# Optimization experiments

Hardware: AMD Instinct MI355X
Metric: run time of the kernel (lower is better)

Reference implementation:

```python
import jax, jax.numpy as jnp
import numpy as np

B, S, D, H = 2, 2048, 512, 8
DK = D // H  # 64


def setup_inputs() -> dict:
    key = jax.random.key(0)
    ks = jax.random.split(key, 16)
    def t(k):
        return jax.random.normal(k, (B, S, D), dtype=jnp.float32)
    inp = {
        'query_real': t(ks[0]), 'key_real': t(ks[1]), 'value_real': t(ks[2]),
        'query_phase': t(ks[3]), 'key_phase': t(ks[4]), 'value_phase': t(ks[5]),
        'mask': jax.random.randint(ks[6], (B, 1, S), 0, 2, dtype=jnp.int32),
    }
    # Four distinct linear layers (clones deepcopies); real and phase paths share them.
    for i, nm in enumerate(['q', 'k', 'v', 'o']):
        inp['W' + nm] = jax.random.normal(ks[7 + 2 * i], (D, D), dtype=jnp.float32) * 0.02
        inp['b' + nm] = jax.random.normal(ks[8 + 2 * i], (D,), dtype=jnp.float32) * 0.02
    return inp


def _lin(x, W, b):
    # nn.Linear: x @ W.T + b
    return jnp.einsum('bsd,ed->bse', x, W) + b


def _heads(x):
    # [B,S,D] -> [B,H,S,DK]
    return jnp.swapaxes(x.reshape(B, S, H, DK), 1, 2)


def reference(query_real, key_real, value_real, query_phase, key_phase, value_phase,
              mask, Wq, bq, Wk, bk, Wv, bv, Wo, bo):
    qr = _heads(_lin(query_real, Wq, bq)); qp = _heads(_lin(query_phase, Wq, bq))
    kr = _heads(_lin(key_real, Wk, bk));   kp = _heads(_lin(key_phase, Wk, bk))
    vr = _heads(_lin(value_real, Wv, bv)); vp = _heads(_lin(value_phase, Wv, bv))

    # complex QK^T: 4 matmuls -> real/imag parts, magnitude score
    sr = jnp.einsum('bhqd,bhkd->bhqk', qr, kr) - jnp.einsum('bhqd,bhkd->bhqk', qp, kp)
    sp = jnp.einsum('bhqd,bhkd->bhqk', qr, kp) + jnp.einsum('bhqd,bhkd->bhqk', qp, kr)
    scores = jnp.sqrt(sr * sr + sp * sp) / jnp.sqrt(jnp.float32(DK))
    # mask [B,1,S] -> unsqueeze head dim -> [B,1,1,S]
    scores = jnp.where(mask[:, None] == 0, jnp.float32(-1e9), scores)
    p = jax.nn.softmax(scores, axis=-1)

    xr = jnp.einsum('bhqk,bhkd->bhqd', p, vr)
    xp = jnp.einsum('bhqk,bhkd->bhqd', p, vp)
    xr = jnp.swapaxes(xr, 1, 2).reshape(B, S, D)
    xp = jnp.swapaxes(xp, 1, 2).reshape(B, S, D)
    return _lin(xr, Wo, bo), _lin(xp, Wo, bo)
```

## Files before the change

### kernel.cpp

```cpp
#include <hip/hip_runtime.h>

typedef __bf16 bf16;
typedef __bf16 bf16x8 __attribute__((ext_vector_type(8)));
typedef float  f32x4  __attribute__((ext_vector_type(4)));

static constexpr int CB = 2;
static constexpr int CS = 2048;
static constexpr int CD = 512;
static constexpr int CH = 8;
static constexpr int CDK = 64;
static constexpr int NROWS = CB * CH * CS;
static constexpr size_t NT = (size_t)CB * CS * CD;
static constexpr size_t WN = (size_t)CD * CD;

__device__ __forceinline__ f32x4 mfma16(bf16x8 a, bf16x8 b, f32x4 c) {
    return __builtin_amdgcn_mfma_f32_16x16x32_bf16(a, b, c, 0, 0, 0);
}

__device__ __forceinline__ bf16x8 cvt8(const float* __restrict__ p) {
    float4 x0 = *reinterpret_cast<const float4*>(p);
    float4 x1 = *reinterpret_cast<const float4*>(p + 4);
    bf16x8 r;
    r[0] = (bf16)x0.x; r[1] = (bf16)x0.y; r[2] = (bf16)x0.z; r[3] = (bf16)x0.w;
    r[4] = (bf16)x1.x; r[5] = (bf16)x1.y; r[6] = (bf16)x1.z; r[7] = (bf16)x1.w;
    return r;
}

__device__ __forceinline__ void gload16(const void* g, void* l) {
    __builtin_amdgcn_global_load_lds(
        (const __attribute__((address_space(1))) void*)g,
        (__attribute__((address_space(3))) void*)l, 16, 0, 0);
}

struct CvtP {
    const float* src[10];
    bf16* dst[10];
    int n8[10];
};
__global__ __launch_bounds__(256) void cvt_kernel(CvtP C) {
    const int t = blockIdx.y;
    const int i = blockIdx.x * 256 + threadIdx.x;
    if (i < C.n8[t])
        *reinterpret_cast<bf16x8*>(C.dst[t] + (size_t)i * 8) =
            cvt8(C.src[t] + (size_t)i * 8);
}

struct PB {
    const bf16* A[6];
    const bf16* W[6];
    const float* bias[6];
    bf16* dst[6];
    int mode[6];
};
__global__ __launch_bounds__(256) void projb_kernel(PB P) {
    __shared__ uint4 tile[2][2][512];

    const int z = blockIdx.z;
    const bf16* __restrict__ A = P.A[z];
    const bf16* __restrict__ W = P.W[z];
    const float* __restrict__ bias = P.bias[z];
    bf16* __restrict__ dst = P.dst[z];
    const int mode = P.mode[z];

    const int m0 = blockIdx.x * 64, n0 = blockIdx.y * 64;
    const int tid = threadIdx.x;
    const int lane = tid & 63, w = tid >> 6;
    const int wm = w >> 1, wn = w & 1;
    const int l16 = lane & 15, lhi = lane >> 4;

    const int tensor = w >> 1, half = w & 1;
    const int rlo = lane >> 3, slotL = lane & 7;
    const bf16* gbase = tensor ? W : A;
    const int t0 = tensor ? n0 : m0;
    const char* gp = (const char*)gbase
                   + (size_t)(t0 + half*32 + rlo) * (CD * 2)
                   + (size_t)((slotL ^ rlo) * 16);

    auto stage = [&](int buf, int kk) {
        const char* p = gp + (size_t)kk * 128;
        uint4* ld = &tile[buf][tensor][half * 256];
        #pragma unroll
        for (int i = 0; i < 4; ++i)
            gload16(p + (size_t)i * 8 * (CD * 2), ld + i * 64);
    };

    f32x4 acc[2][2] = {};

    stage(0, 0);
    asm volatile("s_waitcnt vmcnt(0)" ::: "memory");
    __syncthreads();

    for (int kk = 0; kk < 8; ++kk) {
        if (kk + 1 < 8) stage((kk + 1) & 1, kk + 1);

        const uint4* aT = &tile[kk & 1][0][0];
        const uint4* bT = &tile[kk & 1][1][0];
        #pragma unroll
        for (int ks = 0; ks < 2; ++ks) {
            const int c = ks*4 + lhi;
            const int ra0 = wm*32 + l16, ra1 = ra0 + 16;
            const int rb0 = wn*32 + l16, rb1 = rb0 + 16;
            bf16x8 af0 = __builtin_bit_cast(bf16x8, aT[ra0*8 + (c ^ (ra0 & 7))]);
            bf16x8 af1 = __builtin_bit_cast(bf16x8, aT[ra1*8 + (c ^ (ra1 & 7))]);
            bf16x8 bg0 = __builtin_bit_cast(bf16x8, bT[rb0*8 + (c ^ (rb0 & 7))]);
            bf16x8 bg1 = __builtin_bit_cast(bf16x8, bT[rb1*8 + (c ^ (rb1 & 7))]);
            acc[0][0] = mfma16(af0, bg0, acc[0][0]);
            acc[0][1] = mfma16(af0, bg1, acc[0][1]);
            acc[1][0] = mfma16(af1, bg0, acc[1][0]);
            acc[1][1] = mfma16(af1, bg1, acc[1][1]);
        }
        if (kk + 1 < 8) __syncthreads();
    }

    #pragma unroll
    for (int ms = 0; ms < 2; ++ms)
    #pragma unroll
    for (int ns = 0; ns < 2; ++ns) {
        const int col = n0 + wn*32 + ns*16 + l16;
        const float bv = bias[col];
        const int hh = col >> 6, dk = col & 63;
        #pragma unroll
        for (int i = 0; i < 4; ++i) {
            const int m = m0 + wm*32 + ms*16 + lhi*4 + i;
            const float v = acc[ms][ns][i] + bv;
            const int b = m >> 11, s = m & 2047;
            if (mode == 0)
                dst[(((size_t)(b*CH + hh)) * CS + s) * CDK + dk] = (bf16)v;
            else
                dst[(((size_t)(b*CH + hh)) * CDK + dk) * CS + s] = (bf16)v;
        }
    }
}

__global__ __launch_bounds__(256) void oprojb_kernel(
    const bf16* __restrict__ Xr, const bf16* __restrict__ Xp,
    const bf16* __restrict__ Wo, const float* __restrict__ bo,
    float* __restrict__ out)
{
    __shared__ uint4 tile[2][2][512];

    const bf16* __restrict__ A = blockIdx.z ? Xp : Xr;
    float* __restrict__ dst = out + (size_t)blockIdx.z * NT;

    const int m0 = blockIdx.x * 64, n0 = blockIdx.y * 64;
    const int tid = threadIdx.x;
    const int lane = tid & 63, w = tid >> 6;
    const int wm = w >> 1, wn = w & 1;
    const int l16 = lane & 15, lhi = lane >> 4;

    const int tensor = w >> 1, half = w & 1;
    const int rlo = lane >> 3, slotL = lane & 7;
    const bf16* gbase = tensor ? Wo : A;
    const int t0 = tensor ? n0 : m0;
    const char* gp = (const char*)gbase
                   + (size_t)(t0 + half*32 + rlo) * (CD * 2)
                   + (size_t)((slotL ^ rlo) * 16);

    auto stage = [&](int buf, int kk) {
        const char* p = gp + (size_t)kk * 128;
        uint4* ld = &tile[buf][tensor][half * 256];
        #pragma unroll
        for (int i = 0; i < 4; ++i)
            gload16(p + (size_t)i * 8 * (CD * 2), ld + i * 64);
    };

    f32x4 acc[2][2] = {};

    stage(0, 0);
    asm volatile("s_waitcnt vmcnt(0)" ::: "memory");
    __syncthreads();

    for (int kk = 0; kk < 8; ++kk) {
        if (kk + 1 < 8) stage((kk + 1) & 1, kk + 1);

        const uint4* aT = &tile[kk & 1][0][0];
        const uint4* bT = &tile[kk & 1][1][0];
        #pragma unroll
        for (int ks = 0; ks < 2; ++ks) {
            const int c = ks*4 + lhi;
            const int ra0 = wm*32 + l16, ra1 = ra0 + 16;
            const int rb0 = wn*32 + l16, rb1 = rb0 + 16;
            bf16x8 af0 = __builtin_bit_cast(bf16x8, aT[ra0*8 + (c ^ (ra0 & 7))]);
            bf16x8 af1 = __builtin_bit_cast(bf16x8, aT[ra1*8 + (c ^ (ra1 & 7))]);
            bf16x8 bg0 = __builtin_bit_cast(bf16x8, bT[rb0*8 + (c ^ (rb0 & 7))]);
            bf16x8 bg1 = __builtin_bit_cast(bf16x8, bT[rb1*8 + (c ^ (rb1 & 7))]);
            acc[0][0] = mfma16(af0, bg0, acc[0][0]);
            acc[0][1] = mfma16(af0, bg1, acc[0][1]);
            acc[1][0] = mfma16(af1, bg0, acc[1][0]);
            acc[1][1] = mfma16(af1, bg1, acc[1][1]);
        }
        if (kk + 1 < 8) __syncthreads();
    }

    #pragma unroll
    for (int ms = 0; ms < 2; ++ms)
    #pragma unroll
    for (int ns = 0; ns < 2; ++ns) {
        const int col = n0 + wn*32 + ns*16 + l16;
        const float bv = bo[col];
        #pragma unroll
        for (int i = 0; i < 4; ++i) {
            const int m = m0 + wm*32 + ms*16 + lhi*4 + i;
            dst[(size_t)m * 512 + col] = acc[ms][ns][i] + bv;
        }
    }
}

__global__ __launch_bounds__(256) void attn_kernel(
    const bf16* __restrict__ Qr, const bf16* __restrict__ Qp,
    const bf16* __restrict__ Kr, const bf16* __restrict__ Kp,
    const bf16* __restrict__ Vtr, const bf16* __restrict__ Vtp,
    const int* __restrict__ mask, int lognsp,
    float* __restrict__ POR, float* __restrict__ POP, float* __restrict__ PLs)
{
    __shared__ uint4 stg[2][4][512];
    __shared__ bf16 pL[4][32][64];

    const int F = blockIdx.x;
    const int qt = (F >> 3) & 15;
    const int g  = (F & 7) | ((F >> 7) << 3);
    const int bh = g >> lognsp, z = g & ((1 << lognsp) - 1);
    const int Lkv = CS >> lognsp, kvbase = z * Lkv;
    const int nt = Lkv >> 6;
    const int b = bh >> 3;
    const size_t base = (size_t)bh * CS * CDK;

    const int tid = threadIdx.x, lane = tid & 63, w = tid >> 6;
    const int l16 = lane & 15, lhi = lane >> 4;
    const int q0 = qt * 128 + w * 32;

    const int srowL = lane >> 3, slotL = lane & 7;
    const int chunkL = slotL ^ srowL;
    const char* gsrc;
    size_t laneoff, iStride, tStride;
    if (w == 0)      gsrc = (const char*)Kr;
    else if (w == 1) gsrc = (const char*)Kp;
    else if (w == 2) gsrc = (const char*)Vtr;
    else             gsrc = (const char*)Vtp;
    if (w < 2) {
        laneoff = base*2 + (size_t)(kvbase + srowL) * 128 + chunkL*16;
        iStride = 1024;  tStride = 8192;
    } else {
        laneoff = base*2 + (size_t)srowL * (CS*2) + (size_t)kvbase*2 + chunkL*16;
        iStride = 8 * CS * 2;  tStride = 128;
    }
    const char* gp = gsrc + laneoff;

    auto stage = [&](int bi, int t) {
        const char* p = gp + (size_t)t * tStride;
        uint4* ldst = &stg[bi][w][0];
        #pragma unroll
        for (int i = 0; i < 8; ++i)
            gload16(p + i*iStride, ldst + i*64);
    };

    stage(0, 0);

    bf16x8 qrf[2][2], qpf[2][2], qnf[2][2];
    #pragma unroll
    for (int ms = 0; ms < 2; ++ms)
        #pragma unroll
        for (int ks = 0; ks < 2; ++ks) {
            const size_t qoff = base + (size_t)(q0 + ms*16 + l16) * CDK + ks*32 + lhi*8;
            qrf[ms][ks] = *reinterpret_cast<const bf16x8*>(&Qr[qoff]);
            qpf[ms][ks] = *reinterpret_cast<const bf16x8*>(&Qp[qoff]);
            uint4 t = __builtin_bit_cast(uint4, qpf[ms][ks]);
            t.x ^= 0x80008000u; t.y ^= 0x80008000u; t.z ^= 0x80008000u; t.w ^= 0x80008000u;
            qnf[ms][ks] = __builtin_bit_cast(bf16x8, t);
        }

    unsigned long long keep4[2] = {0ull, 0ull};
    for (int t = 0; t < nt; ++t) {
        const unsigned long long m64 =
            __ballot(mask[b*CS + kvbase + t*64 + lane] != 0);
        const unsigned long long bits = m64 >> l16;
        const unsigned long long nib =
            (bits & 1ull) | ((bits >> 15) & 2ull) | ((bits >> 30) & 4ull) | ((bits >> 45) & 8ull);
        keep4[t >> 4] |= nib << ((t & 15) * 4);
    }

    f32x4 oR[2][4] = {}, oP[2][4] = {};
    float lpart[2][4] = {};

    auto fswz = [](int r) { return (r & 7) ^ (((r >> 3) & 1) << 1); };

    asm volatile("s_waitcnt vmcnt(0)" ::: "memory");
    __syncthreads();

    for (int t = 0; t < nt; ++t) {
        if (t + 1 < nt) stage((t + 1) & 1, t + 1);

        const int bi = t & 1;
        const unsigned int k4 = (unsigned int)(keep4[t >> 4] >> ((t & 15) * 4)) & 0xFu;
        const uint4* kTr = &stg[bi][0][0];
        const uint4* kTp = &stg[bi][1][0];
        const uint4* vTr = &stg[bi][2][0];
        const uint4* vTp = &stg[bi][3][0];

        float sc[2][4][4];
        #pragma unroll
        for (int kb = 0; kb < 4; ++kb) {
            const int krow = kb*16 + l16;
            bf16x8 kr8[2], kp8[2];
            #pragma unroll
            for (int ks = 0; ks < 2; ++ks) {
                const int ci = krow*8 + ((ks*4 + lhi) ^ (krow & 7));
                kr8[ks] = __builtin_bit_cast(bf16x8, kTr[ci]);
                kp8[ks] = __builtin_bit_cast(bf16x8, kTp[ci]);
            }
            const unsigned int keep = (k4 >> kb) & 1u;
            #pragma unroll
            for (int ms = 0; ms < 2; ++ms) {
                f32x4 aR = {}, aP = {};
                __builtin_amdgcn_s_setprio(1);
                #pragma unroll
                for (int ks = 0; ks < 2; ++ks) {
                    aR = mfma16(qrf[ms][ks], kr8[ks], aR);
                    aR = mfma16(qnf[ms][ks], kp8[ks], aR);
                    aP = mfma16(qrf[ms][ks], kp8[ks], aP);
                    aP = mfma16(qpf[ms][ks], kr8[ks], aP);
                }
                __builtin_amdgcn_s_setprio(0);
                #pragma unroll
                for (int i = 0; i < 4; ++i) {
                    const float sr = aR[i], sp = aP[i];
                    const float mag = __builtin_amdgcn_sqrtf(fmaf(sr, sr, sp*sp));
                    float p = __builtin_amdgcn_exp2f(fmaf(mag, 0.18033688f, -5.77078016f));
                    p = keep ? p : 0.0f;
                    sc[ms][kb][i] = p;
                    lpart[ms][i] += p;
                }
            }
        }

        bf16* pB = &pL[w][0][0];
        #pragma unroll
        for (int ms = 0; ms < 2; ++ms)
            #pragma unroll
            for (int i = 0; i < 4; ++i) {
                const int row = ms*16 + lhi*4 + i;
                const int sw = fswz(row) << 3;
                #pragma unroll
                for (int kb = 0; kb < 4; ++kb)
                    pB[row*64 + ((kb*16 + l16) ^ sw)] = (bf16)sc[ms][kb][i];
            }
        asm volatile("s_waitcnt lgkmcnt(0)" ::: "memory");
        __builtin_amdgcn_sched_barrier(0);

        const uint4* pW = reinterpret_cast<const uint4*>(&pL[w][0][0]);
        #pragma unroll
        for (int ks = 0; ks < 2; ++ks) {
            bf16x8 pf[2];
            #pragma unroll
            for (int ms = 0; ms < 2; ++ms) {
                const int prow = ms*16 + l16;
                pf[ms] = __builtin_bit_cast(bf16x8, pW[prow*8 + ((ks*4 + lhi) ^ fswz(prow))]);
            }
            __builtin_amdgcn_s_setprio(1);
            #pragma unroll
            for (int d = 0; d < 4; ++d) {
                const int vrow = d*16 + l16;
                const int ci = vrow*8 + ((ks*4 + lhi) ^ (vrow & 7));
                const bf16x8 v8r = __builtin_bit_cast(bf16x8, vTr[ci]);
                const bf16x8 v8p = __builtin_bit_cast(bf16x8, vTp[ci]);
                #pragma unroll
                for (int ms = 0; ms < 2; ++ms) {
                    oR[ms][d] = mfma16(pf[ms], v8r, oR[ms][d]);
                    oP[ms][d] = mfma16(pf[ms], v8p, oP[ms][d]);
                }
            }
            __builtin_amdgcn_s_setprio(0);
        }

        if (t + 1 < nt) __syncthreads();
    }

    #pragma unroll
    for (int ms = 0; ms < 2; ++ms)
        #pragma unroll
        for (int i = 0; i < 4; ++i) {
            float v = lpart[ms][i];
            v += __shfl_xor(v, 1); v += __shfl_xor(v, 2);
            v += __shfl_xor(v, 4); v += __shfl_xor(v, 8);
            lpart[ms][i] = v;
        }
    const int r0 = bh * CS + q0;
    if (l16 == 0) {
        #pragma unroll
        for (int ms = 0; ms < 2; ++ms)
            #pragma unroll
            for (int i = 0; i < 4; ++i)
                PLs[(size_t)z * NROWS + r0 + ms*16 + lhi*4 + i] = lpart[ms][i];
    }
    const size_t zo = (size_t)z * NROWS * 64;
    #pragma unroll
    for (int ms = 0; ms < 2; ++ms)
        #pragma unroll
        for (int d = 0; d < 4; ++d) {
            const int col = d*16 + l16;
            #pragma unroll
            for (int i = 0; i < 4; ++i) {
                const size_t off = zo + (size_t)(r0 + ms*16 + lhi*4 + i) * 64 + col;
                POR[off] = oR[ms][d][i];
                POP[off] = oP[ms][d][i];
            }
        }
}

__global__ __launch_bounds__(256) void merge_kernel(
    const float* __restrict__ POR, const float* __restrict__ POP,
    const float* __restrict__ PLs, int nsp,
    bf16* __restrict__ Xr, bf16* __restrict__ Xp)
{
    const int idx = blockIdx.x * 256 + threadIdx.x;
    const int r = idx >> 4, c0 = (idx & 15) * 4;
    float l = 0.f;
    f32x4 orv = {}, opv = {};
    for (int zz = 0; zz < nsp; ++zz) {
        l += PLs[(size_t)zz * NROWS + r];
        const size_t o = (size_t)zz * NROWS * 64 + (size_t)r * 64 + c0;
        orv += *reinterpret_cast<const f32x4*>(&POR[o]);
        opv += *reinterpret_cast<const f32x4*>(&POP[o]);
    }
    const float inv = 1.f / l;
    const int bh = r >> 11, q = r & 2047;
    const int b = bh >> 3, h = bh & 7;
    const size_t off = ((size_t)(b*CS + q)) * CD + h*CDK + c0;
    bf16 vr[4], vp[4];
    #pragma unroll
    for (int j = 0; j < 4; ++j) { vr[j] = (bf16)(orv[j]*inv); vp[j] = (bf16)(opv[j]*inv); }
    *reinterpret_cast<uint2*>(&Xr[off]) = *reinterpret_cast<const uint2*>(vr);
    *reinterpret_cast<uint2*>(&Xp[off]) = *reinterpret_cast<const uint2*>(vp);
}

extern "C" void kernel_launch(void* const* d_in, const int* in_sizes, int n_in,
                              void* d_out, int out_size, void* d_ws, size_t ws_size,
                              hipStream_t stream) {
    const float* q_r = (const float*)d_in[0];
    const float* k_r = (const float*)d_in[1];
    const float* v_r = (const float*)d_in[2];
    const float* q_p = (const float*)d_in[3];
    const float* k_p = (const float*)d_in[4];
    const float* v_p = (const float*)d_in[5];
    const int*  mask = (const int*)d_in[6];
    const float* Wq = (const float*)d_in[7];  const float* bq = (const float*)d_in[8];
    const float* Wk = (const float*)d_in[9];  const float* bk = (const float*)d_in[10];
    const float* Wv = (const float*)d_in[11]; const float* bv = (const float*)d_in[12];
    const float* Wo = (const float*)d_in[13]; const float* bo = (const float*)d_in[14];
    float* out = (float*)d_out;

    bf16* ws = (bf16*)d_ws;
    bf16* Abf = ws;
    bf16* Wbf = ws + 6 * NT;
    bf16* Qr  = Wbf + 4 * WN;
    bf16 *Qp = Qr + NT, *Kr = Qp + NT, *Kp = Kr + NT;
    bf16 *Vtr = Kp + NT, *Vtp = Vtr + NT;
    bf16 *Xr = Vtp + NT, *Xp = Xr + NT;
    float* POR = (float*)(Xp + NT);

    const size_t fixedB = (14 * NT + 4 * WN) * sizeof(bf16);
    const size_t per_split = (size_t)NROWS * 64 * 4 * 2 + (size_t)NROWS * 4;
    int nsp, lognsp;
    if (ws_size >= fixedB + 2 * per_split) { nsp = 2; lognsp = 1; }
    else                                   { nsp = 1; lognsp = 0; }
    float* POP = POR + (size_t)nsp * NROWS * 64;
    float* PLs = POP + (size_t)nsp * NROWS * 64;

    dim3 blk(256);

    CvtP C;
    C.src[0]=q_r; C.src[1]=q_p; C.src[2]=k_r; C.src[3]=k_p; C.src[4]=v_r; C.src[5]=v_p;
    C.src[6]=Wq;  C.src[7]=Wk;  C.src[8]=Wv;  C.src[9]=Wo;
    for (int i = 0; i < 6; ++i) { C.dst[i] = Abf + (size_t)i * NT; C.n8[i] = (int)(NT / 8); }
    for (int i = 0; i < 4; ++i) { C.dst[6+i] = Wbf + (size_t)i * WN; C.n8[6+i] = (int)(WN / 8); }
    cvt_kernel<<<dim3((unsigned)(NT / 8 / 256), 10), blk, 0, stream>>>(C);

    PB P;
    for (int i = 0; i < 6; ++i) P.A[i] = Abf + (size_t)i * NT;
    P.W[0]=Wbf;      P.W[1]=Wbf;      P.W[2]=Wbf+WN;   P.W[3]=Wbf+WN;
    P.W[4]=Wbf+2*WN; P.W[5]=Wbf+2*WN;
    P.bias[0]=bq; P.bias[1]=bq; P.bias[2]=bk; P.bias[3]=bk; P.bias[4]=bv; P.bias[5]=bv;
    P.dst[0]=Qr; P.dst[1]=Qp; P.dst[2]=Kr; P.dst[3]=Kp; P.dst[4]=Vtr; P.dst[5]=Vtp;
    P.mode[0]=0; P.mode[1]=0; P.mode[2]=0; P.mode[3]=0; P.mode[4]=1; P.mode[5]=1;
    projb_kernel<<<dim3(64, 8, 6), blk, 0, stream>>>(P);

    attn_kernel<<<dim3(256 * nsp), blk, 0, stream>>>(Qr, Qp, Kr, Kp, Vtr, Vtp,
                                                     mask, lognsp, POR, POP, PLs);

    merge_kernel<<<dim3(NROWS * 16 / 256), blk, 0, stream>>>(POR, POP, PLs, nsp, Xr, Xp);

    oprojb_kernel<<<dim3(64, 8, 2), blk, 0, stream>>>(Xr, Xp, Wbf + 3 * WN, bo, out);
}
```

Before: 128.1 us.

## Compute transposed scores to keep P in registers, drop LDS round-trip

Swaps the MFMA operand order so the score tile comes out transposed, with keys along the accumulator rows. The probabilities can then be packed to bf16 and rearranged with permlane swaps straight into the B-operand layout for the PV MFMA, which removes the per-wave LDS staging buffer, its writes and reads, and the lgkmcnt wait. The mask bits are repacked per lane, and the output is now written as vectorized f32x4 stores. In exchange it relies on gfx950-specific permlane swap instructions and inline asm, and K fragments are reloaded from LDS for each ms instead of being reused.

Result: no change. 128.6 us (+0.4%).

```diff
diff --git a/kernel.cpp b/kernel.cpp
--- a/kernel.cpp
+++ b/kernel.cpp
@@ -214,7 +214,6 @@
     float* __restrict__ POR, float* __restrict__ POP, float* __restrict__ PLs)
 {
     __shared__ uint4 stg[2][4][512];
-    __shared__ bf16 pL[4][32][64];
 
     const int F = blockIdx.x;
     const int qt = (F >> 3) & 15;
@@ -269,20 +268,20 @@
             qnf[ms][ks] = __builtin_bit_cast(bf16x8, t);
         }
 
-    unsigned long long keep4[2] = {0ull, 0ull};
+    unsigned long long keepA[8] = {};
     for (int t = 0; t < nt; ++t) {
         const unsigned long long m64 =
             __ballot(mask[b*CS + kvbase + t*64 + lane] != 0);
-        const unsigned long long bits = m64 >> l16;
-        const unsigned long long nib =
-            (bits & 1ull) | ((bits >> 15) & 2ull) | ((bits >> 30) & 4ull) | ((bits >> 45) & 8ull);
-        keep4[t >> 4] |= nib << ((t & 15) * 4);
+        const unsigned long long s = m64 >> (lhi * 4);
+        const unsigned int k16 = (unsigned int)(s & 0xFull)
+                               | ((unsigned int)((s >> 16) & 0xFull) << 4)
+                               | ((unsigned int)((s >> 32) & 0xFull) << 8)
+                               | ((unsigned int)((s >> 48) & 0xFull) << 12);
+        keepA[t >> 2] |= (unsigned long long)k16 << ((t & 3) * 16);
     }
 
     f32x4 oR[2][4] = {}, oP[2][4] = {};
-    float lpart[2][4] = {};
-
-    auto fswz = [](int r) { return (r & 7) ^ (((r >> 3) & 1) << 1); };
+    float lpart[2] = {0.f, 0.f};
 
     asm volatile("s_waitcnt vmcnt(0)" ::: "memory");
     __syncthreads();
@@ -291,34 +290,29 @@
         if (t + 1 < nt) stage((t + 1) & 1, t + 1);
 
         const int bi = t & 1;
-        const unsigned int k4 = (unsigned int)(keep4[t >> 4] >> ((t & 15) * 4)) & 0xFu;
+        const unsigned int k16 = (unsigned int)(keepA[t >> 2] >> ((t & 3) * 16)) & 0xFFFFu;
         const uint4* kTr = &stg[bi][0][0];
         const uint4* kTp = &stg[bi][1][0];
         const uint4* vTr = &stg[bi][2][0];
         const uint4* vTp = &stg[bi][3][0];
 
-        float sc[2][4][4];
-        #pragma unroll
-        for (int kb = 0; kb < 4; ++kb) {
-            const int krow = kb*16 + l16;
-            bf16x8 kr8[2], kp8[2];
+        #pragma unroll
+        for (int ms = 0; ms < 2; ++ms) {
+            float pp[4][4];
             #pragma unroll
-            for (int ks = 0; ks < 2; ++ks) {
-                const int ci = krow*8 + ((ks*4 + lhi) ^ (krow & 7));
-                kr8[ks] = __builtin_bit_cast(bf16x8, kTr[ci]);
-                kp8[ks] = __builtin_bit_cast(bf16x8, kTp[ci]);
-            }
-            const unsigned int keep = (k4 >> kb) & 1u;
-            #pragma unroll
-            for (int ms = 0; ms < 2; ++ms) {
+            for (int kb = 0; kb < 4; ++kb) {
+                const int krow = kb*16 + l16;
                 f32x4 aR = {}, aP = {};
                 __builtin_amdgcn_s_setprio(1);
                 #pragma unroll
                 for (int ks = 0; ks < 2; ++ks) {
-                    aR = mfma16(qrf[ms][ks], kr8[ks], aR);
-                    aR = mfma16(qnf[ms][ks], kp8[ks], aR);
-                    aP = mfma16(qrf[ms][ks], kp8[ks], aP);
-                    aP = mfma16(qpf[ms][ks], kr8[ks], aP);
+                    const int ci = krow*8 + ((ks*4 + lhi) ^ (krow & 7));
+                    const bf16x8 kr8 = __builtin_bit_cast(bf16x8, kTr[ci]);
+                    const bf16x8 kp8 = __builtin_bit_cast(bf16x8, kTp[ci]);
+                    aR = mfma16(kr8, qrf[ms][ks], aR);
+                    aR = mfma16(kp8, qnf[ms][ks], aR);
+                    aP = mfma16(kr8, qpf[ms][ks], aP);
+                    aP = mfma16(kp8, qrf[ms][ks], aP);
                 }
                 __builtin_amdgcn_s_setprio(0);
                 #pragma unroll
@@ -326,84 +320,59 @@
                     const float sr = aR[i], sp = aP[i];
                     const float mag = __builtin_amdgcn_sqrtf(fmaf(sr, sr, sp*sp));
                     float p = __builtin_amdgcn_exp2f(fmaf(mag, 0.18033688f, -5.77078016f));
-                    p = keep ? p : 0.0f;
-                    sc[ms][kb][i] = p;
-                    lpart[ms][i] += p;
+                    p = ((k16 >> (kb*4 + i)) & 1u) ? p : 0.0f;
+                    pp[kb][i] = p;
+                    lpart[ms] += p;
                 }
             }
-        }
-
-        bf16* pB = &pL[w][0][0];
-        #pragma unroll
-        for (int ms = 0; ms < 2; ++ms)
             #pragma unroll
-            for (int i = 0; i < 4; ++i) {
-                const int row = ms*16 + lhi*4 + i;
-                const int sw = fswz(row) << 3;
+            for (int c = 0; c < 2; ++c) {
+                unsigned int r0, r1, r2, r3;
+                asm("v_cvt_pk_bf16_f32 %0, %1, %2" : "=v"(r0) : "v"(pp[2*c][0]),   "v"(pp[2*c][1]));
+                asm("v_cvt_pk_bf16_f32 %0, %1, %2" : "=v"(r1) : "v"(pp[2*c][2]),   "v"(pp[2*c][3]));
+                asm("v_cvt_pk_bf16_f32 %0, %1, %2" : "=v"(r2) : "v"(pp[2*c+1][0]), "v"(pp[2*c+1][1]));
+                asm("v_cvt_pk_bf16_f32 %0, %1, %2" : "=v"(r3) : "v"(pp[2*c+1][2]), "v"(pp[2*c+1][3]));
+                asm volatile("v_permlane32_swap_b32 %0, %1" : "+v"(r0), "+v"(r2));
+                asm volatile("v_permlane32_swap_b32 %0, %1" : "+v"(r1), "+v"(r3));
+                asm volatile("v_permlane16_swap_b32 %0, %1" : "+v"(r0), "+v"(r2));
+                asm volatile("v_permlane16_swap_b32 %0, %1" : "+v"(r1), "+v"(r3));
+                uint4 fw; fw.x = r0; fw.y = r1; fw.z = r2; fw.w = r3;
+                const bf16x8 pa = __builtin_bit_cast(bf16x8, fw);
+                __builtin_amdgcn_s_setprio(1);
                 #pragma unroll
-                for (int kb = 0; kb < 4; ++kb)
-                    pB[row*64 + ((kb*16 + l16) ^ sw)] = (bf16)sc[ms][kb][i];
+                for (int dt = 0; dt < 4; ++dt) {
+                    const int vrow = dt*16 + l16;
+                    const int ci = vrow*8 + ((c*4 + lhi) ^ (vrow & 7));
+                    oR[ms][dt] = mfma16(__builtin_bit_cast(bf16x8, vTr[ci]), pa, oR[ms][dt]);
+                    oP[ms][dt] = mfma16(__builtin_bit_cast(bf16x8, vTp[ci]), pa, oP[ms][dt]);
+                }
+                __builtin_amdgcn_s_setprio(0);
             }
-        asm volatile("s_waitcnt lgkmcnt(0)" ::: "memory");
-        __builtin_amdgcn_sched_barrier(0);
-
-        const uint4* pW = reinterpret_cast<const uint4*>(&pL[w][0][0]);
-        #pragma unroll
-        for (int ks = 0; ks < 2; ++ks) {
-            bf16x8 pf[2];
-            #pragma unroll
-            for (int ms = 0; ms < 2; ++ms) {
-                const int prow = ms*16 + l16;
-                pf[ms] = __builtin_bit_cast(bf16x8, pW[prow*8 + ((ks*4 + lhi) ^ fswz(prow))]);
-            }
-            __builtin_amdgcn_s_setprio(1);
-            #pragma unroll
-            for (int d = 0; d < 4; ++d) {
-                const int vrow = d*16 + l16;
-                const int ci = vrow*8 + ((ks*4 + lhi) ^ (vrow & 7));
-                const bf16x8 v8r = __builtin_bit_cast(bf16x8, vTr[ci]);
-                const bf16x8 v8p = __builtin_bit_cast(bf16x8, vTp[ci]);
-                #pragma unroll
-                for (int ms = 0; ms < 2; ++ms) {
-                    oR[ms][d] = mfma16(pf[ms], v8r, oR[ms][d]);
-                    oP[ms][d] = mfma16(pf[ms], v8p, oP[ms][d]);
-                }
-            }
-            __builtin_amdgcn_s_setprio(0);
         }
 
         if (t + 1 < nt) __syncthreads();
     }
 
     #pragma unroll
+    for (int ms = 0; ms < 2; ++ms) {
+        float v = lpart[ms];
+        v += __shfl_xor(v, 16);
+        v += __shfl_xor(v, 32);
+        lpart[ms] = v;
+    }
+    const int r0q = bh * CS + q0;
+    if (lane < 16) {
+        PLs[(size_t)z * NROWS + r0q + lane]      = lpart[0];
+        PLs[(size_t)z * NROWS + r0q + 16 + lane] = lpart[1];
+    }
+    const size_t zo = (size_t)z * NROWS * 64;
+    #pragma unroll
     for (int ms = 0; ms < 2; ++ms)
         #pragma unroll
-        for (int i = 0; i < 4; ++i) {
-            float v = lpart[ms][i];
-            v += __shfl_xor(v, 1); v += __shfl_xor(v, 2);
-            v += __shfl_xor(v, 4); v += __shfl_xor(v, 8);
-            lpart[ms][i] = v;
-        }
-    const int r0 = bh * CS + q0;
-    if (l16 == 0) {
-        #pragma unroll
-        for (int ms = 0; ms < 2; ++ms)
-            #pragma unroll
-            for (int i = 0; i < 4; ++i)
-                PLs[(size_t)z * NROWS + r0 + ms*16 + lhi*4 + i] = lpart[ms][i];
-    }
-    const size_t zo = (size_t)z * NROWS * 64;
-    #pragma unroll
-    for (int ms = 0; ms < 2; ++ms)
-        #pragma unroll
-        for (int d = 0; d < 4; ++d) {
-            const int col = d*16 + l16;
-            #pragma unroll
-            for (int i = 0; i < 4; ++i) {
-                const size_t off = zo + (size_t)(r0 + ms*16 + lhi*4 + i) * 64 + col;
-                POR[off] = oR[ms][d][i];
-                POP[off] = oP[ms][d][i];
-            }
+        for (int dt = 0; dt < 4; ++dt) {
+            const size_t off = zo + (size_t)(r0q + ms*16 + l16) * 64 + dt*16 + lhi*4;
+            *reinterpret_cast<f32x4*>(&POR[off]) = oR[ms][dt];
+            *reinterpret_cast<f32x4*>(&POP[off]) = oP[ms][dt];
         }
 }
 
```
